# Kernel tuning notes

Hardware: AMD Instinct MI355X
Metric: run time of the kernel (lower is better)

Reference implementation:

```python
import jax, jax.numpy as jnp
import numpy as np

LENGTH_MIN = 5
LENGTH_MAX = 64
EMBED_DIM = 512
POOL_SIZE = 20
TOP_K = 5
BETA = 0.5
LN_EPS = 1e-5
COS_EPS = 1e-8


def setup_inputs() -> dict:
    key = jax.random.key(0)
    ks = jax.random.split(key, 8)
    B, N = 1024, 64
    H = EMBED_DIM // 2
    # xavier-uniform-ish init scale for params
    def xavier(k, shape, fan_in, fan_out):
        lim = float(np.sqrt(6.0 / (fan_in + fan_out)))
        return jax.random.uniform(k, shape, jnp.float32, -lim, lim)
    return {
        "x_embed": jax.random.normal(ks[0], (B, N, EMBED_DIM), jnp.float32),
        "quality_score": jax.random.uniform(ks[1], (B, 1), jnp.float32),
        "prompt_keys": xavier(ks[2], (POOL_SIZE, EMBED_DIM), POOL_SIZE, EMBED_DIM),
        "prompt_embeddings": xavier(ks[3], (POOL_SIZE, LENGTH_MAX, EMBED_DIM), LENGTH_MAX, EMBED_DIM),
        "w1": xavier(ks[4], (1, H), 1, H),
        "b1": jnp.zeros((H,), jnp.float32),
        "ln_g": jnp.ones((H,), jnp.float32),
        "ln_b": jnp.zeros((H,), jnp.float32),
        "w2": xavier(ks[5], (H, EMBED_DIM), H, EMBED_DIM),
        "b2": jnp.zeros((EMBED_DIM,), jnp.float32),
    }


def _quality_proj(q, w1, b1, ln_g, ln_b, w2, b2):
    h = q @ w1 + b1  # [B, H]
    mu = h.mean(-1, keepdims=True)
    var = ((h - mu) ** 2).mean(-1, keepdims=True)
    h = (h - mu) * jax.lax.rsqrt(var + LN_EPS) * ln_g + ln_b
    h = jax.nn.relu(h)
    return h @ w2 + b2  # [B, D]


def reference(x_embed, quality_score, prompt_keys, prompt_embeddings, w1, b1, ln_g, ln_b, w2, b2):
    query = _quality_proj(quality_score, w1, b1, ln_g, ln_b, w2, b2)  # [B, D]
    # cosine similarity vs pool keys
    qn = query / jnp.maximum(jnp.linalg.norm(query, axis=-1, keepdims=True), COS_EPS)
    kn = prompt_keys / jnp.maximum(jnp.linalg.norm(prompt_keys, axis=-1, keepdims=True), COS_EPS)
    sims = qn @ kn.T  # [B, P]
    scale = 1.0 + BETA * quality_score.mean()
    weights = jax.nn.softmax(sims * scale, axis=1)  # [B, P]
    # batched top-k (replaces the per-sample Python loop)
    topk_w, topk_idx = jax.lax.top_k(weights, TOP_K)  # [B, K]
    # per-sample dynamic length -> validity mask over length_max positions
    mu_b = quality_score.mean(axis=1)  # [B]; quality_score[b:b+1].mean()
    len_f = LENGTH_MIN + (LENGTH_MAX - LENGTH_MIN) * (1.0 - mu_b / 5.0)
    lens = jnp.clip(jnp.trunc(len_f).astype(jnp.int32), LENGTH_MIN, LENGTH_MAX)  # [B]
    mask = (jnp.arange(LENGTH_MAX)[None, :] < lens[:, None]).astype(x_embed.dtype)  # [B, L]
    # gather selected prompts and weighted-sum over top_k
    sel = prompt_embeddings[topk_idx]  # [B, K, L, D]
    out = jnp.einsum("bk,bkld->bld", topk_w, sel) * mask[:, :, None]  # [B, L, D]
    return out
```

## Files before the change

### kernel.cpp

```cpp
#include <hip/hip_runtime.h>
#include <hip/hip_bf16.h>
#include <math.h>

#define LENGTH_MIN 5
#define LENGTH_MAX 64
#define EMBED_DIM 512
#define HDIM      256
#define POOL      20
#define TOPK      5
#define BETA      0.5f
#define LN_EPS    1e-5f
#define COS_EPS   1e-8f

typedef float v4f __attribute__((ext_vector_type(4)));


__global__ __launch_bounds__(256) void query_all_kernel(
    const float* __restrict__ quality, const float* __restrict__ keys,
    const float* __restrict__ w1, const float* __restrict__ b1,
    const float* __restrict__ ln_g, const float* __restrict__ ln_b,
    const float* __restrict__ w2, const float* __restrict__ b2,
    float* __restrict__ ws, int B)
{
    __shared__ float red[24];
    __shared__ float invk_s[POOL];
    __shared__ float hn_s[4][HDIM];
    __shared__ float qbuf[4][EMBED_DIM];

    int t = threadIdx.x;
    int wave = t >> 6, lane = t & 63;
    int b0 = blockIdx.x * 4;

    float qpart = 0.f;
    for (int i = t; i < B; i += 256) qpart += quality[i];
    float a = w1[t], c = b1[t];
    float vals[6] = { qpart, a, a * a, c, c * c, a * c };
    #pragma unroll
    for (int i = 0; i < 6; i++) {
        float v = vals[i];
        #pragma unroll
        for (int off = 32; off > 0; off >>= 1) v += __shfl_xor(v, off);
        if (lane == 0) red[i * 4 + wave] = v;
    }
    #pragma unroll
    for (int j = 0; j < 5; j++) {
        int p = wave + 4 * j;
        const float* kp = keys + p * EMBED_DIM;
        float s = 0.f;
        #pragma unroll
        for (int i = 0; i < 8; i++) { float x = kp[lane + 64 * i]; s = fmaf(x, x, s); }
        #pragma unroll
        for (int off = 32; off > 0; off >>= 1) s += __shfl_xor(s, off);
        if (lane == 0) invk_s[p] = 1.f / fmaxf(sqrtf(s), COS_EPS);
    }
    __syncthreads();

    float qmean = (red[0] + red[1] + red[2] + red[3]) / (float)B;
    float mw1   = (red[4] + red[5] + red[6] + red[7]) * (1.f / 256.f);
    float Ew2   = (red[8] + red[9] + red[10] + red[11]) * (1.f / 256.f);
    float mb1   = (red[12] + red[13] + red[14] + red[15]) * (1.f / 256.f);
    float Eb2   = (red[16] + red[17] + red[18] + red[19]) * (1.f / 256.f);
    float Eab   = (red[20] + red[21] + red[22] + red[23]) * (1.f / 256.f);
    float Vw1 = Ew2 - mw1 * mw1;
    float Vb1 = Eb2 - mb1 * mb1;
    float Cv  = Eab - mw1 * mb1;

    float gt = ln_g[t], lbt = ln_b[t];
    float qv4[4];
    #pragma unroll
    for (int bi = 0; bi < 4; bi++) {
        float q = quality[b0 + bi];
        qv4[bi] = q;
        float mu  = q * mw1 + mb1;
        float var = q * q * Vw1 + 2.f * q * Cv + Vb1;
        float inv = rsqrtf(var + LN_EPS);
        float h = q * a + c;
        hn_s[bi][t] = fmaxf((h - mu) * inv * gt + lbt, 0.f);
    }
    __syncthreads();

    int d0 = 2 * t;
    float2 b2v = *(const float2*)(b2 + d0);
    float acc0[4], acc1[4];
    #pragma unroll
    for (int bi = 0; bi < 4; bi++) { acc0[bi] = b2v.x; acc1[bi] = b2v.y; }

    for (int j = 0; j < HDIM; j += 4) {
        float2 wv0 = *(const float2*)(w2 + (j + 0) * EMBED_DIM + d0);
        float2 wv1 = *(const float2*)(w2 + (j + 1) * EMBED_DIM + d0);
        float2 wv2 = *(const float2*)(w2 + (j + 2) * EMBED_DIM + d0);
        float2 wv3 = *(const float2*)(w2 + (j + 3) * EMBED_DIM + d0);
        #pragma unroll
        for (int bi = 0; bi < 4; bi++) {
            float4 hv = *(const float4*)&hn_s[bi][j];
            acc0[bi] = fmaf(hv.x, wv0.x, acc0[bi]);
            acc1[bi] = fmaf(hv.x, wv0.y, acc1[bi]);
            acc0[bi] = fmaf(hv.y, wv1.x, acc0[bi]);
            acc1[bi] = fmaf(hv.y, wv1.y, acc1[bi]);
            acc0[bi] = fmaf(hv.z, wv2.x, acc0[bi]);
            acc1[bi] = fmaf(hv.z, wv2.y, acc1[bi]);
            acc0[bi] = fmaf(hv.w, wv3.x, acc0[bi]);
            acc1[bi] = fmaf(hv.w, wv3.y, acc1[bi]);
        }
    }
    #pragma unroll
    for (int bi = 0; bi < 4; bi++)
        *(float2*)&qbuf[bi][d0] = make_float2(acc0[bi], acc1[bi]);
    __syncthreads();

    int bi = wave;
    float s[POOL + 1];
    #pragma unroll
    for (int p = 0; p <= POOL; p++) s[p] = 0.f;
    #pragma unroll
    for (int i = 0; i < 8; i++) {
        int d = lane + 64 * i;
        float qd = qbuf[bi][d];
        s[POOL] = fmaf(qd, qd, s[POOL]);
        #pragma unroll
        for (int p = 0; p < POOL; p++)
            s[p] = fmaf(qd, keys[p * EMBED_DIM + d], s[p]);
    }
    #pragma unroll
    for (int off = 32; off > 0; off >>= 1) {
        #pragma unroll
        for (int p = 0; p <= POOL; p++) s[p] += __shfl_xor(s[p], off);
    }

    float invq  = 1.f / fmaxf(sqrtf(s[POOL]), COS_EPS);
    float scale = 1.f + BETA * qmean;
    float sim[POOL];
    #pragma unroll
    for (int p = 0; p < POOL; p++) sim[p] = s[p] * invq * invk_s[p] * scale;

    float m = sim[0];
    #pragma unroll
    for (int p = 1; p < POOL; p++) m = fmaxf(m, sim[p]);
    float e[POOL]; float den = 0.f;
    #pragma unroll
    for (int p = 0; p < POOL; p++) { e[p] = expf(sim[p] - m); den += e[p]; }
    float invden = 1.f / den;

    unsigned picked = 0;
    float tw[TOPK]; int ti[TOPK];
    #pragma unroll
    for (int k = 0; k < TOPK; k++) {
        float best = -1.f; int bidx = 0;
        #pragma unroll
        for (int p = 0; p < POOL; p++) {
            bool free_p = ((picked >> p) & 1u) == 0u;
            if (free_p && e[p] > best) { best = e[p]; bidx = p; }
        }
        picked |= (1u << bidx);
        tw[k] = best * invden;
        ti[k] = bidx;
    }

    if (lane == 0) {
        int b = b0 + bi;
        float* topw = ws + 32;
        int*   topi = (int*)(ws + 32) + 5 * B;
        int*   lenp = (int*)(ws + 32) + 10 * B;
        #pragma unroll
        for (int k = 0; k < TOPK; k++) {
            topw[b * TOPK + k] = tw[k];
            topi[b * TOPK + k] = ti[k];
        }
        float q = qv4[bi];
        float lf = __fadd_rn(5.f, __fmul_rn(59.f, __fsub_rn(1.f, __fdiv_rn(q, 5.f))));
        int len = (int)truncf(lf);
        len = min(max(len, LENGTH_MIN), LENGTH_MAX);
        lenp[b] = len;
    }
}

__global__ __launch_bounds__(256) void scatter_kernel(
    const float* __restrict__ pe, const float* __restrict__ ws,
    float* __restrict__ out, int B)
{
    int b  = blockIdx.x >> 3;
    int l0 = (blockIdx.x & 7) * 8;
    const float* topw = ws + 32;
    const int*   topi = (const int*)(ws + 32) + 5 * B;
    const int*   lenp = (const int*)(ws + 32) + 10 * B;

    float w[TOPK]; int idx[TOPK];
    #pragma unroll
    for (int k = 0; k < TOPK; k++) {
        w[k]   = topw[b * TOPK + k];
        idx[k] = topi[b * TOPK + k];
    }
    int len = lenp[b];

    int t = threadIdx.x;
    #pragma unroll
    for (int sweep = 0; sweep < 4; sweep++) {
        int l  = l0 + sweep * 2 + (t >> 7);
        int d4 = (t & 127) * 4;
        v4f r = { 0.f, 0.f, 0.f, 0.f };
        if (l < len) {
            #pragma unroll
            for (int k = 0; k < TOPK; k++) {
                v4f pv = *(const v4f*)(pe + (idx[k] * 64 + l) * EMBED_DIM + d4);
                r += pv * w[k];
            }
        }
        __builtin_nontemporal_store(r, (v4f*)(out + ((size_t)(b * 64 + l)) * EMBED_DIM + d4));
    }
}

extern "C" void kernel_launch(void* const* d_in, const int* in_sizes, int n_in,
                              void* d_out, int out_size, void* d_ws, size_t ws_size,
                              hipStream_t stream) {
    const float* quality = (const float*)d_in[1];
    const float* keys    = (const float*)d_in[2];
    const float* pe      = (const float*)d_in[3];
    const float* w1      = (const float*)d_in[4];
    const float* b1      = (const float*)d_in[5];
    const float* ln_g    = (const float*)d_in[6];
    const float* ln_b    = (const float*)d_in[7];
    const float* w2      = (const float*)d_in[8];
    const float* b2      = (const float*)d_in[9];
    float* out = (float*)d_out;
    float* ws  = (float*)d_ws;
    int B = in_sizes[1];

    query_all_kernel<<<B / 4, 256, 0, stream>>>(quality, keys, w1, b1, ln_g, ln_b,
                                                w2, b2, ws, B);
    scatter_kernel<<<B * 8, 256, 0, stream>>>(pe, ws, out, B);
}
```

Before: 274.2 us.

## Use dense pool weights and keep prompt rows in registers across batch

The query kernel now writes a dense 20-entry weight vector per sample, with zeros for unselected prompts, in place of top-k indices and weights. The scatter kernel is restructured so each block owns one sequence position and 64 samples. It loads all 20 prompt rows for that position into registers once, then computes every sample's output as a dense weighted sum. This removes the gather of prompt_embeddings per sample, at the cost of 4x more FMAs, higher register pressure and fewer, smaller blocks (1024 blocks of 128 threads).

```diff
diff --git a/kernel.cpp b/kernel.cpp
--- a/kernel.cpp
+++ b/kernel.cpp
@@ -142,7 +142,6 @@
     float invden = 1.f / den;
 
     unsigned picked = 0;
-    float tw[TOPK]; int ti[TOPK];
     #pragma unroll
     for (int k = 0; k < TOPK; k++) {
         float best = -1.f; int bidx = 0;
@@ -152,20 +151,15 @@
             if (free_p && e[p] > best) { best = e[p]; bidx = p; }
         }
         picked |= (1u << bidx);
-        tw[k] = best * invden;
-        ti[k] = bidx;
     }
 
     if (lane == 0) {
         int b = b0 + bi;
-        float* topw = ws + 32;
-        int*   topi = (int*)(ws + 32) + 5 * B;
-        int*   lenp = (int*)(ws + 32) + 10 * B;
-        #pragma unroll
-        for (int k = 0; k < TOPK; k++) {
-            topw[b * TOPK + k] = tw[k];
-            topi[b * TOPK + k] = ti[k];
-        }
+        float* Wd   = ws + 32;
+        int*   lenp = (int*)(ws + 32 + 32 * B);
+        #pragma unroll
+        for (int p = 0; p < POOL; p++)
+            Wd[b * 32 + p] = ((picked >> p) & 1u) ? e[p] * invden : 0.f;
         float q = qv4[bi];
         float lf = __fadd_rn(5.f, __fmul_rn(59.f, __fsub_rn(1.f, __fdiv_rn(q, 5.f))));
         int len = (int)truncf(lf);
@@ -174,38 +168,36 @@
     }
 }
 
-__global__ __launch_bounds__(256) void scatter_kernel(
+__global__ __launch_bounds__(128) void scatter_kernel(
     const float* __restrict__ pe, const float* __restrict__ ws,
     float* __restrict__ out, int B)
 {
-    int b  = blockIdx.x >> 3;
-    int l0 = (blockIdx.x & 7) * 8;
-    const float* topw = ws + 32;
-    const int*   topi = (const int*)(ws + 32) + 5 * B;
-    const int*   lenp = (const int*)(ws + 32) + 10 * B;
-
-    float w[TOPK]; int idx[TOPK];
-    #pragma unroll
-    for (int k = 0; k < TOPK; k++) {
-        w[k]   = topw[b * TOPK + k];
-        idx[k] = topi[b * TOPK + k];
-    }
-    int len = lenp[b];
-
-    int t = threadIdx.x;
-    #pragma unroll
-    for (int sweep = 0; sweep < 4; sweep++) {
-        int l  = l0 + sweep * 2 + (t >> 7);
-        int d4 = (t & 127) * 4;
+    int l     = blockIdx.x & 63;
+    int chunk = blockIdx.x >> 6;
+    int b0    = chunk * 64;
+    int d4    = threadIdx.x * 4;
+
+    const float* Wd   = ws + 32;
+    const int*   lenp = (const int*)(ws + 32 + 32 * B);
+
+    v4f pv[POOL];
+    #pragma unroll
+    for (int p = 0; p < POOL; p++)
+        pv[p] = *(const v4f*)(pe + (p * 64 + l) * EMBED_DIM + d4);
+
+    float* orow = out + (size_t)(b0 * 64 + l) * EMBED_DIM + d4;
+    #pragma unroll 4
+    for (int bi = 0; bi < 64; bi++) {
+        int b = b0 + bi;
+        float msk = (l < lenp[b]) ? 1.f : 0.f;
+        const float* wrow = Wd + b * 32;
         v4f r = { 0.f, 0.f, 0.f, 0.f };
-        if (l < len) {
-            #pragma unroll
-            for (int k = 0; k < TOPK; k++) {
-                v4f pv = *(const v4f*)(pe + (idx[k] * 64 + l) * EMBED_DIM + d4);
-                r += pv * w[k];
-            }
-        }
-        __builtin_nontemporal_store(r, (v4f*)(out + ((size_t)(b * 64 + l)) * EMBED_DIM + d4));
+        #pragma unroll
+        for (int p = 0; p < POOL; p++)
+            r += pv[p] * wrow[p];
+        r *= msk;
+        __builtin_nontemporal_store(r, (v4f*)orow);
+        orow += (size_t)64 * EMBED_DIM;
     }
 }
 
@@ -227,5 +219,5 @@
 
     query_all_kernel<<<B / 4, 256, 0, stream>>>(quality, keys, w1, b1, ln_g, ln_b,
                                                 w2, b2, ws, B);
-    scatter_kernel<<<B * 8, 256, 0, stream>>>(pe, ws, out, B);
+    scatter_kernel<<<(B / 64) * 64, 128, 0, stream>>>(pe, ws, out, B);
 }
```

Result: no change. 275.9 us (+0.6%).
